# Performance work log

Hardware: AMD Instinct MI355X
Metric: run time of the kernel (lower is better)

Reference implementation:

```python
import jax, jax.numpy as jnp
import numpy as np

# dims: 3 bert layers averaged, B batch, T_SUB subword tokens (excl. CLS), W words, D=768 bert dim
B, T_SUB, W, D = 64, 512, 256, 768
H = 20          # lstm_hidden
CAP_DIM = 10
CAP_TYPES = 4
IN_DIM = D + CAP_DIM


def setup_inputs() -> dict:
    key = jax.random.key(0)
    ks = jax.random.split(key, 10)
    hiddens = jax.random.normal(ks[0], (3, B, T_SUB + 1, D), jnp.float32)  # [CLS] at pos 0
    # nondecreasing word ids, each word gets exactly T_SUB//W subwords (all segments non-empty)
    bert2toks = jnp.tile(jnp.repeat(jnp.arange(W), T_SUB // W)[None, :], (B, 1)).astype(jnp.int32)
    cap_inds = jax.random.randint(ks[1], (B, W), 0, CAP_TYPES)
    cap_table = jax.random.normal(ks[2], (CAP_TYPES, CAP_DIM), jnp.float32) * 0.1
    s = 1.0 / np.sqrt(H)
    u = lambda k, shp: jax.random.uniform(k, shp, jnp.float32, -s, s)
    w_ih_f = u(ks[3], (4 * H, IN_DIM))
    w_hh_f = u(ks[4], (4 * H, H))
    b_f = u(ks[5], (4 * H,))  # b_ih + b_hh fused
    w_ih_b = u(ks[6], (4 * H, IN_DIM))
    w_hh_b = u(ks[7], (4 * H, H))
    b_b = u(ks[8], (4 * H,))
    return {"hiddens": hiddens, "bert2toks": bert2toks, "cap_inds": cap_inds,
            "cap_table": cap_table, "w_ih_f": w_ih_f, "w_hh_f": w_hh_f, "b_f": b_f,
            "w_ih_b": w_ih_b, "w_hh_b": w_hh_b, "b_b": b_b}


def _lstm_dir(xs, w_ih, w_hh, b, reverse):
    # xs: [B, W, IN_DIM] -> hs: [B, W, H]
    xs_t = jnp.swapaxes(xs, 0, 1)  # [W, B, IN]
    if reverse:
        xs_t = xs_t[::-1]
    h0 = jnp.zeros((xs.shape[0], H), xs.dtype)

    def step(carry, xt):
        h, c = carry
        g = xt @ w_ih.T + h @ w_hh.T + b  # [B, 4H], pytorch gate order i,f,g,o
        i, f, gg, o = jnp.split(g, 4, axis=-1)
        c = jax.nn.sigmoid(f) * c + jax.nn.sigmoid(i) * jnp.tanh(gg)
        h = jax.nn.sigmoid(o) * jnp.tanh(c)
        return (h, c), h

    _, hs = jax.lax.scan(step, (h0, h0), xs_t)
    if reverse:
        hs = hs[::-1]
    return jnp.swapaxes(hs, 0, 1)


def reference(hiddens, bert2toks, cap_inds, cap_table,
              w_ih_f, w_hh_f, b_f, w_ih_b, w_hh_b, b_b):
    # mean over the 3 selected bert layers
    means = jnp.mean(hiddens, axis=0)          # [B, T_SUB+1, D]
    sub = means[:, 1:T_SUB + 1]                # skip [CLS]: means[i+1] indexing
    # ragged subword->word mean pooling as a segment mean
    flat_ids = (bert2toks + jnp.arange(B, dtype=bert2toks.dtype)[:, None] * W).reshape(-1)
    sums = jax.ops.segment_sum(sub.reshape(B * T_SUB, D), flat_ids, num_segments=B * W)
    cnts = jax.ops.segment_sum(jnp.ones((B * T_SUB, 1), sub.dtype), flat_ids, num_segments=B * W)
    word_h = (sums / cnts).reshape(B, W, D)
    cap_emb = cap_table[cap_inds]              # [B, W, CAP_DIM]
    x = jnp.concatenate([word_h, cap_emb], axis=-1)  # [B, W, IN_DIM]
    out = jnp.concatenate([
        _lstm_dir(x, w_ih_f, w_hh_f, b_f, False),
        _lstm_dir(x, w_ih_b, w_hh_b, b_b, True),
    ], axis=-1)                                # [B, W, 2H]
    return out
```

## Files before the change

kernel.cpp:

```cpp
#include <hip/hip_runtime.h>
#include <math.h>

#define BB 64
#define T_SUB 512
#define WW 256
#define DD 768
#define HH 20
#define CAP_DIM 10
#define IN_DIM 778
#define KPAD 800
#define G4 80
#define NOUT 160

typedef _Float16 f16x8 __attribute__((ext_vector_type(8)));
typedef float f32x4 __attribute__((ext_vector_type(4)));
typedef unsigned int uint2v __attribute__((ext_vector_type(2)));

#define WP_OFF   ((size_t)0)
#define SEG_OFF  ((size_t)256000)
#define X_OFF    ((size_t)387072)

__global__ __launch_bounds__(256) void k_prep(
    const float* __restrict__ wf, const float* __restrict__ wb,
    const int* __restrict__ b2t,
    _Float16* __restrict__ wp, int2* __restrict__ seg)
{
    int blk = blockIdx.x;
    if (blk < NOUT) {
        int j = blk;
        const float* src = (j < G4) ? (wf + (size_t)j * IN_DIM)
                                    : (wb + (size_t)(j - G4) * IN_DIM);
        for (int k = threadIdx.x; k < KPAD; k += 256)
            wp[(size_t)j * KPAD + k] = (k < IN_DIM) ? (_Float16)src[k] : (_Float16)0.f;
    } else {
        int b = blk - NOUT, w = threadIdx.x;
        const int* row = b2t + (size_t)b * T_SUB;
        int lo = 0, hi = T_SUB;
        while (lo < hi) { int m = (lo + hi) >> 1; if (row[m] < w) lo = m + 1; else hi = m; }
        int lo2 = lo, hi2 = T_SUB;
        while (lo2 < hi2) { int m = (lo2 + hi2) >> 1; if (row[m] < w + 1) lo2 = m + 1; else hi2 = m; }
        seg[(size_t)b * WW + w] = make_int2(lo, lo2 - lo);
    }
}

__global__ __launch_bounds__(256) void k_mean(
    const float* __restrict__ hiddens, const int2* __restrict__ seg,
    const int* __restrict__ cap_inds, const float* __restrict__ cap_table,
    _Float16* __restrict__ x)
{
    int idx = blockIdx.x * 256 + threadIdx.x;
    int d2 = idx % 50;
    int bw = idx / 50;
    int b = bw >> 8;
    int2 sg = seg[bw];
    int lo = sg.x, cnt = sg.y;
    const size_t LSTR = (size_t)BB * (T_SUB + 1) * DD;
    const float* rowp = hiddens + ((size_t)b * (T_SUB + 1) + lo + 1) * DD;
    float inv = 1.0f / (3.0f * (float)(cnt > 0 ? cnt : 1));
    bool bmean = (d2 + 50) < 96;
    f16x8 ra, rb;

    if (cnt == 2 && bmean) {
        const float* pa  = rowp + d2 * 8;
        const float* pb_ = rowp + (d2 + 50) * 8;
        float4 A0 = *(const float4*)(pa);                float4 A1 = *(const float4*)(pa + 4);
        float4 A2 = *(const float4*)(pa + DD);           float4 A3 = *(const float4*)(pa + DD + 4);
        float4 A4 = *(const float4*)(pa + LSTR);         float4 A5 = *(const float4*)(pa + LSTR + 4);
        float4 A6 = *(const float4*)(pa + LSTR + DD);    float4 A7 = *(const float4*)(pa + LSTR + DD + 4);
        float4 A8 = *(const float4*)(pa + 2*LSTR);       float4 A9 = *(const float4*)(pa + 2*LSTR + 4);
        float4 Aa = *(const float4*)(pa + 2*LSTR + DD);  float4 Ab = *(const float4*)(pa + 2*LSTR + DD + 4);
        float4 B0 = *(const float4*)(pb_);               float4 B1 = *(const float4*)(pb_ + 4);
        float4 B2 = *(const float4*)(pb_ + DD);          float4 B3 = *(const float4*)(pb_ + DD + 4);
        float4 B4 = *(const float4*)(pb_ + LSTR);        float4 B5 = *(const float4*)(pb_ + LSTR + 4);
        float4 B6 = *(const float4*)(pb_ + LSTR + DD);   float4 B7 = *(const float4*)(pb_ + LSTR + DD + 4);
        float4 B8 = *(const float4*)(pb_ + 2*LSTR);      float4 B9 = *(const float4*)(pb_ + 2*LSTR + 4);
        float4 Ba = *(const float4*)(pb_ + 2*LSTR + DD); float4 Bb = *(const float4*)(pb_ + 2*LSTR + DD + 4);
        ra[0] = (_Float16)((A0.x+A2.x+A4.x+A6.x+A8.x+Aa.x) * inv);
        ra[1] = (_Float16)((A0.y+A2.y+A4.y+A6.y+A8.y+Aa.y) * inv);
        ra[2] = (_Float16)((A0.z+A2.z+A4.z+A6.z+A8.z+Aa.z) * inv);
        ra[3] = (_Float16)((A0.w+A2.w+A4.w+A6.w+A8.w+Aa.w) * inv);
        ra[4] = (_Float16)((A1.x+A3.x+A5.x+A7.x+A9.x+Ab.x) * inv);
        ra[5] = (_Float16)((A1.y+A3.y+A5.y+A7.y+A9.y+Ab.y) * inv);
        ra[6] = (_Float16)((A1.z+A3.z+A5.z+A7.z+A9.z+Ab.z) * inv);
        ra[7] = (_Float16)((A1.w+A3.w+A5.w+A7.w+A9.w+Ab.w) * inv);
        rb[0] = (_Float16)((B0.x+B2.x+B4.x+B6.x+B8.x+Ba.x) * inv);
        rb[1] = (_Float16)((B0.y+B2.y+B4.y+B6.y+B8.y+Ba.y) * inv);
        rb[2] = (_Float16)((B0.z+B2.z+B4.z+B6.z+B8.z+Ba.z) * inv);
        rb[3] = (_Float16)((B0.w+B2.w+B4.w+B6.w+B8.w+Ba.w) * inv);
        rb[4] = (_Float16)((B1.x+B3.x+B5.x+B7.x+B9.x+Bb.x) * inv);
        rb[5] = (_Float16)((B1.y+B3.y+B5.y+B7.y+B9.y+Bb.y) * inv);
        rb[6] = (_Float16)((B1.z+B3.z+B5.z+B7.z+B9.z+Bb.z) * inv);
        rb[7] = (_Float16)((B1.w+B3.w+B5.w+B7.w+B9.w+Bb.w) * inv);
    } else {
        float a[8], bacc[8];
#pragma unroll
        for (int q = 0; q < 8; q++) { a[q] = 0.f; bacc[q] = 0.f; }
        for (int l = 0; l < 3; ++l)
            for (int ti = 0; ti < cnt; ++ti) {
                const float* p = rowp + l * LSTR + (size_t)ti * DD;
                float4 v0 = *(const float4*)(p + d2 * 8);
                float4 v1 = *(const float4*)(p + d2 * 8 + 4);
                a[0]+=v0.x; a[1]+=v0.y; a[2]+=v0.z; a[3]+=v0.w;
                a[4]+=v1.x; a[5]+=v1.y; a[6]+=v1.z; a[7]+=v1.w;
                if (bmean) {
                    float4 u0 = *(const float4*)(p + (d2 + 50) * 8);
                    float4 u1 = *(const float4*)(p + (d2 + 50) * 8 + 4);
                    bacc[0]+=u0.x; bacc[1]+=u0.y; bacc[2]+=u0.z; bacc[3]+=u0.w;
                    bacc[4]+=u1.x; bacc[5]+=u1.y; bacc[6]+=u1.z; bacc[7]+=u1.w;
                }
            }
#pragma unroll
        for (int q = 0; q < 8; q++) { ra[q] = (_Float16)(a[q] * inv); rb[q] = (_Float16)(bacc[q] * inv); }
    }
    if (!bmean) {
        int ci = cap_inds[bw];
#pragma unroll
        for (int q = 0; q < 8; q++) {
            int c = (d2 + 50 - 96) * 8 + q;
            rb[q] = (c < CAP_DIM) ? (_Float16)cap_table[ci * CAP_DIM + c] : (_Float16)0.f;
        }
    }
    *(f16x8*)(x + (size_t)bw * KPAD + d2 * 8) = ra;
    *(f16x8*)(x + (size_t)bw * KPAD + (d2 + 50) * 8) = rb;
}

__device__ __forceinline__ float xchg32(float v) {
    unsigned int a = __float_as_uint(v);
    uint2v r = __builtin_amdgcn_permlane32_swap(a, a, false, false);
    return __uint_as_float(r[0] ^ r[1] ^ a);
}

__global__ __launch_bounds__(320) void k_lstm(
    const _Float16* __restrict__ x, const _Float16* __restrict__ wp,
    const float* __restrict__ bias_f, const float* __restrict__ bias_b,
    const float* __restrict__ whh_f, const float* __restrict__ whh_b,
    float* __restrict__ out)
{
    __shared__ float gbuf[2][64 * G4];
    int dir  = blockIdx.x >> 6;
    int b    = blockIdx.x & 63;
    int t    = threadIdx.x;
    int wv   = t >> 6;
    int lane = t & 63;

    int mtile = wv - 1;
    int col   = lane & 15;
    int koff  = (lane >> 4) * 8;
    const _Float16* bp = wp + (size_t)(dir * G4 + col) * KPAD + koff;
    float bias_v[5];
    if (wv > 0) {
#pragma unroll
        for (int nf = 0; nf < 5; nf++)
            bias_v[nf] = (dir ? bias_b : bias_f)[nf * 16 + col];
    }

    const float* whh = dir ? whh_b : whh_f;
    int j = lane & 31; if (j > 19) j = 19;
    bool low = lane < 32;
    float mm = low ? 1.f : 2.f;
    float aa = low ? 0.f : -1.f;
    int coff = low ? (40 + 2 * j) : (2 * j);
    float w0[HH], w1[HH];
    if (wv == 0) {
        int r0 = low ? (20 + j) : j;
        int r1 = low ? (60 + j) : (40 + j);
#pragma unroll
        for (int k = 0; k < HH; k++) {
            w0[k] = whh[r0 * HH + k];
            w1[k] = whh[r1 * HH + k];
        }
    }

#define COMPUTE_CHUNK(CH, BUF) do {                                             \
    int base_w = dir ? (192 - (CH) * 64) : (CH) * 64;                           \
    int arow = b * 256 + base_w + mtile * 16 + (lane & 15);                     \
    const _Float16* ap = x + (size_t)arow * KPAD + koff;                        \
    f32x4 acc[5];                                                               \
    _Pragma("unroll")                                                           \
    for (int nf = 0; nf < 5; nf++)                                              \
        _Pragma("unroll")                                                       \
        for (int r = 0; r < 4; r++) acc[nf][r] = 0.f;                           \
    for (int k0 = 0; k0 < KPAD; k0 += 32) {                                     \
        f16x8 af = *(const f16x8*)(ap + k0);                                    \
        _Pragma("unroll")                                                       \
        for (int nf = 0; nf < 5; nf++) {                                        \
            f16x8 bf = *(const f16x8*)(bp + (size_t)nf * 16 * KPAD + k0);       \
            acc[nf] = __builtin_amdgcn_mfma_f32_16x16x32_f16(af, bf, acc[nf], 0, 0, 0); \
        }                                                                       \
    }                                                                           \
    int lrow = mtile * 16 + (lane >> 4) * 4;                                    \
    _Pragma("unroll")                                                           \
    for (int nf = 0; nf < 5; nf++) {                                            \
        int g = nf * 16 + col;                                                  \
        int pcol = (g % 40) * 2 + (g / 40);                                     \
        _Pragma("unroll")                                                       \
        for (int r = 0; r < 4; r++)                                             \
            gbuf[BUF][(lrow + r) * G4 + pcol] = acc[nf][r] + bias_v[nf];        \
    }                                                                           \
} while (0)

    if (wv > 0) COMPUTE_CHUNK(0, 0);
    __syncthreads();

    float h = 0.f, c = 0.f;
    int w = dir ? (WW - 1) : 0;
    int stepd = dir ? -1 : 1;

    for (int ch = 0; ch < 4; ++ch) {
        int cb = ch & 1;
        if (wv > 0) {
            if (ch + 1 < 4) COMPUTE_CHUNK(ch + 1, cb ^ 1);
        } else {
            __builtin_amdgcn_s_setprio(1);
            int base = dir ? (192 - ch * 64) : ch * 64;
            float2 pre = *(const float2*)(&gbuf[cb][(w - base) * G4 + coff]);
            for (int sl = 0; sl < 64; ++sl) {
                int wn = w + stepd;
                float2 nxt = make_float2(0.f, 0.f);
                if (sl < 63)
                    nxt = *(const float2*)(&gbuf[cb][(wn - base) * G4 + coff]);
                float a0a = pre.x, a0b = 0.f, a1a = pre.y, a1b = 0.f;
#pragma unroll
                for (int k = 0; k < 10; k++) {
                    float hk  = __uint_as_float(__builtin_amdgcn_readlane(__float_as_uint(h), k));
                    float hk2 = __uint_as_float(__builtin_amdgcn_readlane(__float_as_uint(h), k + 10));
                    a0a = fmaf(hk,  w0[k],      a0a);
                    a1a = fmaf(hk,  w1[k],      a1a);
                    a0b = fmaf(hk2, w0[k + 10], a0b);
                    a1b = fmaf(hk2, w1[k + 10], a1b);
                }
                float a0 = a0a + a0b, a1 = a1a + a1b;
                float u0 = 1.f / (1.f + __expf(-a0));
                float uu = 1.f / (1.f + __expf(-mm * a1));
                float u1 = fmaf(uu, mm, aa);
                float p  = u0 * u1;
                float ps = xchg32(p);
                c = fmaf(u0, c, ps);
                float tc = fmaf(2.f, 1.f / (1.f + __expf(-2.f * c)), -1.f);
                h = u1 * tc;
                if (lane < HH)
                    out[((size_t)b * WW + w) * (2 * HH) + dir * HH + lane] = h;
                pre = nxt;
                w = wn;
            }
            __builtin_amdgcn_s_setprio(0);
        }
        __syncthreads();
    }
#undef COMPUTE_CHUNK
}

extern "C" void kernel_launch(void* const* d_in, const int* in_sizes, int n_in,
                              void* d_out, int out_size, void* d_ws, size_t ws_size,
                              hipStream_t stream) {
    const float* hiddens   = (const float*)d_in[0];
    const int*   bert2toks = (const int*)d_in[1];
    const int*   cap_inds  = (const int*)d_in[2];
    const float* cap_table = (const float*)d_in[3];
    const float* w_ih_f    = (const float*)d_in[4];
    const float* w_hh_f    = (const float*)d_in[5];
    const float* b_f       = (const float*)d_in[6];
    const float* w_ih_b    = (const float*)d_in[7];
    const float* w_hh_b    = (const float*)d_in[8];
    const float* b_b       = (const float*)d_in[9];
    float* out = (float*)d_out;

    _Float16* wpad = (_Float16*)((char*)d_ws + WP_OFF);
    int2*     seg  = (int2*)((char*)d_ws + SEG_OFF);
    _Float16* x    = (_Float16*)((char*)d_ws + X_OFF);

    k_prep<<<NOUT + BB, 256, 0, stream>>>(w_ih_f, w_ih_b, bert2toks, wpad, seg);
    k_mean<<<(BB * WW * 50) / 256, 256, 0, stream>>>(hiddens, seg, cap_inds, cap_table, x);
    k_lstm<<<128, 320, 0, stream>>>(x, wpad, b_f, b_b, w_hh_f, w_hh_b, out);
}
```

Before: 160.2 us.

## Precompute all input gates in fp16 LDS before serial LSTM recurrence

Replaces the chunked double-buffered overlap with a single upfront phase: four MFMA waves each compute the input projection for 64 words, reusing B fragments across four M tiles, and store all 256 words' gate pre-activations as fp16 in shared memory. The recurrent wave then runs all 256 steps without per-chunk barriers. LOG2E is folded into the weights and bias so exp2f replaces expf. This trades GEMM/recurrence overlap for barrier-free recurrence and better B-fragment reuse, and storing gates in fp16 adds rounding error. The GEMM waves return early after a __syncthreads, which leaves the barrier behaviour unusual.

Result: faster. 156.2 us (-2.5%).

```diff
diff --git a/kernel.cpp b/kernel.cpp
--- a/kernel.cpp
+++ b/kernel.cpp
@@ -11,6 +11,7 @@
 #define KPAD 800
 #define G4 80
 #define NOUT 160
+#define LOG2E 1.44269504f
 
 typedef _Float16 f16x8 __attribute__((ext_vector_type(8)));
 typedef float f32x4 __attribute__((ext_vector_type(4)));
@@ -31,7 +32,8 @@
         const float* src = (j < G4) ? (wf + (size_t)j * IN_DIM)
                                     : (wb + (size_t)(j - G4) * IN_DIM);
         for (int k = threadIdx.x; k < KPAD; k += 256)
-            wp[(size_t)j * KPAD + k] = (k < IN_DIM) ? (_Float16)src[k] : (_Float16)0.f;
+            wp[(size_t)j * KPAD + k] = (k < IN_DIM) ? (_Float16)(LOG2E * src[k])
+                                                    : (_Float16)0.f;
     } else {
         int b = blk - NOUT, w = threadIdx.x;
         const int* row = b2t + (size_t)b * T_SUB;
@@ -136,22 +138,57 @@
     const float* __restrict__ whh_f, const float* __restrict__ whh_b,
     float* __restrict__ out)
 {
-    __shared__ float gbuf[2][64 * G4];
+    __shared__ _Float16 gb[WW * G4];
     int dir  = blockIdx.x >> 6;
     int b    = blockIdx.x & 63;
     int t    = threadIdx.x;
     int wv   = t >> 6;
     int lane = t & 63;
 
-    int mtile = wv - 1;
-    int col   = lane & 15;
-    int koff  = (lane >> 4) * 8;
-    const _Float16* bp = wp + (size_t)(dir * G4 + col) * KPAD + koff;
-    float bias_v[5];
-    if (wv > 0) {
+    if (wv >= 1) {
+        int col  = lane & 15;
+        int koff = (lane >> 4) * 8;
+        int wbase = (wv - 1) * 64;
+        const _Float16* bp = wp + (size_t)(dir * G4 + col) * KPAD + koff;
+        float bias_v[5];
 #pragma unroll
         for (int nf = 0; nf < 5; nf++)
-            bias_v[nf] = (dir ? bias_b : bias_f)[nf * 16 + col];
+            bias_v[nf] = LOG2E * (dir ? bias_b : bias_f)[nf * 16 + col];
+        f32x4 acc[4][5];
+#pragma unroll
+        for (int mt = 0; mt < 4; mt++)
+#pragma unroll
+            for (int nf = 0; nf < 5; nf++)
+#pragma unroll
+                for (int r = 0; r < 4; r++) acc[mt][nf][r] = 0.f;
+        for (int k0 = 0; k0 < KPAD; k0 += 32) {
+            f16x8 bf[5];
+#pragma unroll
+            for (int nf = 0; nf < 5; nf++)
+                bf[nf] = *(const f16x8*)(bp + (size_t)nf * 16 * KPAD + k0);
+#pragma unroll
+            for (int mt = 0; mt < 4; mt++) {
+                int arow = b * 256 + wbase + mt * 16 + (lane & 15);
+                f16x8 af = *(const f16x8*)(x + (size_t)arow * KPAD + koff + k0);
+#pragma unroll
+                for (int nf = 0; nf < 5; nf++)
+                    acc[mt][nf] = __builtin_amdgcn_mfma_f32_16x16x32_f16(af, bf[nf], acc[mt][nf], 0, 0, 0);
+            }
+        }
+#pragma unroll
+        for (int mt = 0; mt < 4; mt++)
+#pragma unroll
+            for (int nf = 0; nf < 5; nf++) {
+                int g = nf * 16 + col;
+                int pcol = (g % 40) * 2 + (g / 40);
+#pragma unroll
+                for (int r = 0; r < 4; r++) {
+                    int word = wbase + mt * 16 + (lane >> 4) * 4 + r;
+                    gb[word * G4 + pcol] = (_Float16)(acc[mt][nf][r] + bias_v[nf]);
+                }
+            }
+        __syncthreads();
+        return;
     }
 
     const float* whh = dir ? whh_b : whh_f;
@@ -161,93 +198,57 @@
     float aa = low ? 0.f : -1.f;
     int coff = low ? (40 + 2 * j) : (2 * j);
     float w0[HH], w1[HH];
-    if (wv == 0) {
+    {
         int r0 = low ? (20 + j) : j;
         int r1 = low ? (60 + j) : (40 + j);
 #pragma unroll
         for (int k = 0; k < HH; k++) {
-            w0[k] = whh[r0 * HH + k];
-            w1[k] = whh[r1 * HH + k];
-        }
-    }
-
-#define COMPUTE_CHUNK(CH, BUF) do {                                             \
-    int base_w = dir ? (192 - (CH) * 64) : (CH) * 64;                           \
-    int arow = b * 256 + base_w + mtile * 16 + (lane & 15);                     \
-    const _Float16* ap = x + (size_t)arow * KPAD + koff;                        \
-    f32x4 acc[5];                                                               \
-    _Pragma("unroll")                                                           \
-    for (int nf = 0; nf < 5; nf++)                                              \
-        _Pragma("unroll")                                                       \
-        for (int r = 0; r < 4; r++) acc[nf][r] = 0.f;                           \
-    for (int k0 = 0; k0 < KPAD; k0 += 32) {                                     \
-        f16x8 af = *(const f16x8*)(ap + k0);                                    \
-        _Pragma("unroll")                                                       \
-        for (int nf = 0; nf < 5; nf++) {                                        \
-            f16x8 bf = *(const f16x8*)(bp + (size_t)nf * 16 * KPAD + k0);       \
-            acc[nf] = __builtin_amdgcn_mfma_f32_16x16x32_f16(af, bf, acc[nf], 0, 0, 0); \
-        }                                                                       \
-    }                                                                           \
-    int lrow = mtile * 16 + (lane >> 4) * 4;                                    \
-    _Pragma("unroll")                                                           \
-    for (int nf = 0; nf < 5; nf++) {                                            \
-        int g = nf * 16 + col;                                                  \
-        int pcol = (g % 40) * 2 + (g / 40);                                     \
-        _Pragma("unroll")                                                       \
-        for (int r = 0; r < 4; r++)                                             \
-            gbuf[BUF][(lrow + r) * G4 + pcol] = acc[nf][r] + bias_v[nf];        \
-    }                                                                           \
-} while (0)
-
-    if (wv > 0) COMPUTE_CHUNK(0, 0);
+            w0[k] = LOG2E * whh[r0 * HH + k];
+            w1[k] = LOG2E * whh[r1 * HH + k];
+        }
+    }
     __syncthreads();
 
+    __builtin_amdgcn_s_setprio(1);
+    const float TCM = -2.f * LOG2E;
     float h = 0.f, c = 0.f;
     int w = dir ? (WW - 1) : 0;
     int stepd = dir ? -1 : 1;
 
-    for (int ch = 0; ch < 4; ++ch) {
-        int cb = ch & 1;
-        if (wv > 0) {
-            if (ch + 1 < 4) COMPUTE_CHUNK(ch + 1, cb ^ 1);
-        } else {
-            __builtin_amdgcn_s_setprio(1);
-            int base = dir ? (192 - ch * 64) : ch * 64;
-            float2 pre = *(const float2*)(&gbuf[cb][(w - base) * G4 + coff]);
-            for (int sl = 0; sl < 64; ++sl) {
-                int wn = w + stepd;
-                float2 nxt = make_float2(0.f, 0.f);
-                if (sl < 63)
-                    nxt = *(const float2*)(&gbuf[cb][(wn - base) * G4 + coff]);
-                float a0a = pre.x, a0b = 0.f, a1a = pre.y, a1b = 0.f;
-#pragma unroll
-                for (int k = 0; k < 10; k++) {
-                    float hk  = __uint_as_float(__builtin_amdgcn_readlane(__float_as_uint(h), k));
-                    float hk2 = __uint_as_float(__builtin_amdgcn_readlane(__float_as_uint(h), k + 10));
-                    a0a = fmaf(hk,  w0[k],      a0a);
-                    a1a = fmaf(hk,  w1[k],      a1a);
-                    a0b = fmaf(hk2, w0[k + 10], a0b);
-                    a1b = fmaf(hk2, w1[k + 10], a1b);
-                }
-                float a0 = a0a + a0b, a1 = a1a + a1b;
-                float u0 = 1.f / (1.f + __expf(-a0));
-                float uu = 1.f / (1.f + __expf(-mm * a1));
-                float u1 = fmaf(uu, mm, aa);
-                float p  = u0 * u1;
-                float ps = xchg32(p);
-                c = fmaf(u0, c, ps);
-                float tc = fmaf(2.f, 1.f / (1.f + __expf(-2.f * c)), -1.f);
-                h = u1 * tc;
-                if (lane < HH)
-                    out[((size_t)b * WW + w) * (2 * HH) + dir * HH + lane] = h;
-                pre = nxt;
-                w = wn;
-            }
-            __builtin_amdgcn_s_setprio(0);
-        }
-        __syncthreads();
-    }
-#undef COMPUTE_CHUNK
+    union { unsigned int u; _Float16 hx[2]; } cu;
+    cu.u = *(const unsigned int*)(gb + w * G4 + coff);
+    float2 pre = make_float2((float)cu.hx[0], (float)cu.hx[1]);
+
+    for (int sl = 0; sl < WW; ++sl) {
+        int wn = w + stepd;
+        int wnc = wn < 0 ? 0 : (wn > 255 ? 255 : wn);
+        union { unsigned int u; _Float16 hx[2]; } nu;
+        nu.u = *(const unsigned int*)(gb + wnc * G4 + coff);
+        float a0a = pre.x, a0b = 0.f, a1a = pre.y, a1b = 0.f;
+#pragma unroll
+        for (int k = 0; k < 10; k++) {
+            float hk  = __uint_as_float(__builtin_amdgcn_readlane(__float_as_uint(h), k));
+            float hk2 = __uint_as_float(__builtin_amdgcn_readlane(__float_as_uint(h), k + 10));
+            a0a = fmaf(hk,  w0[k],      a0a);
+            a1a = fmaf(hk,  w1[k],      a1a);
+            a0b = fmaf(hk2, w0[k + 10], a0b);
+            a1b = fmaf(hk2, w1[k + 10], a1b);
+        }
+        float a0 = a0a + a0b, a1 = a1a + a1b;
+        float u0 = 1.f / (1.f + exp2f(-a0));
+        float uu = 1.f / (1.f + exp2f(-mm * a1));
+        float u1 = fmaf(uu, mm, aa);
+        float p  = u0 * u1;
+        float ps = xchg32(p);
+        c = fmaf(u0, c, ps);
+        float tc = fmaf(2.f, 1.f / (1.f + exp2f(TCM * c)), -1.f);
+        h = u1 * tc;
+        if (lane < HH)
+            out[((size_t)b * WW + w) * (2 * HH) + dir * HH + lane] = h;
+        pre = make_float2((float)nu.hx[0], (float)nu.hx[1]);
+        w = wn;
+    }
+    __builtin_amdgcn_s_setprio(0);
 }
 
 extern "C" void kernel_launch(void* const* d_in, const int* in_sizes, int n_in,
```
